# Kernel optimization log

Measured on AMD Instinct MI355X. Metric: run time of the kernel, lower is better.

The kernel has to match this reference:

```python
import jax, jax.numpy as jnp
import numpy as np

N = 100_000   # total nodes across all subgraphs in batch
E = 1_600_000 # edges (avg degree 16)
B = 1_000     # number of subgraphs
D = 128       # in_dim = out_dim
SZ = N // B   # nodes per subgraph


def setup_inputs() -> dict:
    key = jax.random.key(0)
    ks = jax.random.split(key, 8)
    feat = jax.random.normal(ks[0], (N, D), dtype=jnp.float32)
    edge_src = jax.random.randint(ks[1], (E,), 0, N, dtype=jnp.int32)
    edge_dst = jax.random.randint(ks[2], (E,), 0, N, dtype=jnp.int32)
    # pre-normalized edge weights (is_normed=True path)
    edge_w = jax.random.uniform(ks[3], (E,), dtype=jnp.float32)
    s = 1.0 / np.sqrt(D)
    W1 = jax.random.normal(ks[4], (D, D), dtype=jnp.float32) * s
    W2 = jax.random.normal(ks[5], (D, D), dtype=jnp.float32) * s
    Wp = jax.random.normal(ks[6], (D, D), dtype=jnp.float32) * s
    b1 = jnp.zeros((D,), jnp.float32)
    b2 = jnp.zeros((D,), jnp.float32)
    bp = jnp.zeros((D,), jnp.float32)
    # contiguous equal-size subgraphs; target = first node of each subgraph
    seg_ids = jnp.repeat(jnp.arange(B, dtype=jnp.int32), SZ)
    target = jnp.arange(B, dtype=jnp.int32) * SZ
    size_subg = jnp.full((B,), float(SZ), jnp.float32)
    return dict(feat=feat, edge_w=edge_w, W1=W1, b1=b1, W2=W2, b2=b2,
                Wp=Wp, bp=bp, size_subg=size_subg,
                edge_src=edge_src, edge_dst=edge_dst,
                seg_ids=seg_ids, target=target)


def _gcn_layer(x, src, dst, w, W, b):
    # sparse A_hat @ x : gather src features, weight, scatter-add into dst
    msg = x[src] * w[:, None]                       # [E, D]
    agg = jax.ops.segment_sum(msg, dst, num_segments=N)  # [N, D]
    return jax.nn.relu(agg @ W + b)


def reference(feat, edge_w, W1, b1, W2, b2, Wp, bp, size_subg,
              edge_src, edge_dst, seg_ids, target):
    # two stacked GCN layers (self.structure = [structure1, structure2])
    h1 = _gcn_layer(feat, edge_src, edge_dst, edge_w, W1, b1)
    h2 = _gcn_layer(h1, edge_src, edge_dst, edge_w, W2, b2)
    # ResPool: residual-sum over layer outputs, mean pool per subgraph,
    # add target-node embedding (residual), then linear + relu
    h = h1 + h2                                              # [N, D]
    pooled = jax.ops.segment_sum(h, seg_ids, num_segments=B)
    pooled = pooled / size_subg[:, None] + h[target]         # [B, D]
    emb = jax.nn.relu(pooled @ Wp + bp)
    # F.normalize(p=2, dim=1), eps=1e-12
    norm = jnp.sqrt(jnp.sum(emb * emb, axis=1, keepdims=True))
    emb = emb / jnp.maximum(norm, 1e-12)
    return emb  # EnsembleDummy just returns the single branch
```

## Files before the change

### kernel.cpp

```cpp
#include <hip/hip_runtime.h>

#define DD 128
#define CHUNK 4096
#define BSH 8
#define MAXBK 512
#define MAXCH 512
#define CAP 6144

typedef _Float16 half8 __attribute__((ext_vector_type(8)));
typedef _Float16 half4v __attribute__((ext_vector_type(4)));
typedef float floatx4 __attribute__((ext_vector_type(4)));
typedef float floatx2 __attribute__((ext_vector_type(2)));

__global__ __launch_bounds__(256) void k_prep(const float* __restrict__ W1,
                                              _Float16* __restrict__ W1t,
                                              const float* __restrict__ W2,
                                              _Float16* __restrict__ W2t) {
    int idx = blockIdx.x * 256 + threadIdx.x;
    const float* W = (idx < DD * DD) ? W1 : W2;
    _Float16* Wt = (idx < DD * DD) ? W1t : W2t;
    int id = idx & (DD * DD - 1);
    int n = id >> 7, k = id & 127;
    Wt[n * DD + k] = (_Float16)W[k * DD + n];
}

__global__ __launch_bounds__(512) void k_histg1(const int* __restrict__ dst,
                                                int* __restrict__ histT,
                                                int E, int nChunks,
                                                const float* __restrict__ A,
                                                const _Float16* __restrict__ Wt,
                                                unsigned char* __restrict__ Y, int nrows) {
    if (blockIdx.x < nChunks) {
        __shared__ int lhist[MAXBK];
        int tid = threadIdx.x;
        lhist[tid] = 0;
        __syncthreads();
        int beg = blockIdx.x * CHUNK;
        int end = min(beg + CHUNK, E);
        for (int k = beg + tid; k < end; k += 512)
            atomicAdd(&lhist[dst[k] >> BSH], 1);
        __syncthreads();
        histT[tid * MAXCH + blockIdx.x] = lhist[tid];
    } else {
        int gblk = blockIdx.x - nChunks;
        int wave = threadIdx.x >> 6;
        int lane = threadIdx.x & 63;
        int row0 = gblk * 256 + wave * 32;
        int m = lane & 15;
        int q = lane >> 4;
        int r0 = min(row0 + m, nrows - 1);
        int r1 = min(row0 + 16 + m, nrows - 1);

        floatx4 acc[2][8];
        #pragma unroll
        for (int t = 0; t < 2; ++t)
            #pragma unroll
            for (int c = 0; c < 8; ++c)
                acc[t][c] = (floatx4){0.f, 0.f, 0.f, 0.f};

        #pragma unroll
        for (int ks = 0; ks < 4; ++ks) {
            int kbase = ks * 32 + q * 8;
            float4 x0 = *reinterpret_cast<const float4*>(A + (size_t)r0 * DD + kbase);
            float4 x1 = *reinterpret_cast<const float4*>(A + (size_t)r0 * DD + kbase + 4);
            float4 y0 = *reinterpret_cast<const float4*>(A + (size_t)r1 * DD + kbase);
            float4 y1 = *reinterpret_cast<const float4*>(A + (size_t)r1 * DD + kbase + 4);
            half8 a0, a1;
            a0[0]=(_Float16)x0.x; a0[1]=(_Float16)x0.y; a0[2]=(_Float16)x0.z; a0[3]=(_Float16)x0.w;
            a0[4]=(_Float16)x1.x; a0[5]=(_Float16)x1.y; a0[6]=(_Float16)x1.z; a0[7]=(_Float16)x1.w;
            a1[0]=(_Float16)y0.x; a1[1]=(_Float16)y0.y; a1[2]=(_Float16)y0.z; a1[3]=(_Float16)y0.w;
            a1[4]=(_Float16)y1.x; a1[5]=(_Float16)y1.y; a1[6]=(_Float16)y1.z; a1[7]=(_Float16)y1.w;
            #pragma unroll
            for (int c = 0; c < 8; ++c) {
                half8 b = *reinterpret_cast<const half8*>(Wt + (size_t)(c * 16 + m) * DD + kbase);
                acc[0][c] = __builtin_amdgcn_mfma_f32_16x16x32_f16(b, a0, acc[0][c], 0, 0, 0);
                acc[1][c] = __builtin_amdgcn_mfma_f32_16x16x32_f16(b, a1, acc[1][c], 0, 0, 0);
            }
        }

        #pragma unroll
        for (int t = 0; t < 2; ++t) {
            int row = row0 + t * 16 + m;
            if (row >= nrows) continue;
            size_t rb = (size_t)row * DD;
            #pragma unroll
            for (int c = 0; c < 8; ++c) {
                int col = c * 16 + q * 4;
                int u = 0;
                u = __builtin_amdgcn_cvt_pk_fp8_f32(acc[t][c][0], acc[t][c][1], u, false);
                u = __builtin_amdgcn_cvt_pk_fp8_f32(acc[t][c][2], acc[t][c][3], u, true);
                *reinterpret_cast<unsigned int*>(&Y[rb + col]) = (unsigned int)u;
            }
        }
    }
}

__global__ __launch_bounds__(512) void k_scan(int* __restrict__ histT,
                                              int* __restrict__ gcur, int nChunks) {
    __shared__ int wsum[8];
    int b = blockIdx.x;
    int c = threadIdx.x;
    int v = (c < nChunks) ? histT[b * MAXCH + c] : 0;
    int lane = c & 63, wave = c >> 6;
    int inc = v;
    #pragma unroll
    for (int off = 1; off < 64; off <<= 1) {
        int t = __shfl_up(inc, off, 64);
        if (lane >= off) inc += t;
    }
    if (lane == 63) wsum[wave] = inc;
    __syncthreads();
    if (c == 0) {
        int run = 0;
        #pragma unroll
        for (int j = 0; j < 8; ++j) { int t = wsum[j]; wsum[j] = run; run += t; }
    }
    __syncthreads();
    int ex = inc - v + wsum[wave];
    if (c < nChunks) histT[b * MAXCH + c] = ex;
    if (c == nChunks - 1) gcur[b] = ex + v;
}

__global__ __launch_bounds__(512) void k_pass1(const int* __restrict__ src,
                                               const int* __restrict__ dst,
                                               const float* __restrict__ w,
                                               const int* __restrict__ histT,
                                               int2* __restrict__ out, int E, int NB) {
    __shared__ int2 stg[CHUNK];
    __shared__ unsigned short bok[CHUNK];
    __shared__ int lhist[MAXBK];
    __shared__ int loff[MAXBK];
    __shared__ int lbase[MAXBK];
    __shared__ int lcur[MAXBK];
    int tid = threadIdx.x;
    lhist[tid] = 0;
    __syncthreads();

    int beg = blockIdx.x * CHUNK;
    int end = min(beg + CHUNK, E);
    for (int k = beg + tid; k < end; k += 512)
        atomicAdd(&lhist[dst[k] >> BSH], 1);
    __syncthreads();
    if (tid < 64) {
        int base = tid * 8, v[8], s = 0;
        #pragma unroll
        for (int j = 0; j < 8; ++j) { v[j] = lhist[base + j]; s += v[j]; }
        int scn = s;
        #pragma unroll
        for (int off = 1; off < 64; off <<= 1) {
            int t = __shfl_up(scn, off, 64);
            if (tid >= off) scn += t;
        }
        int ex = scn - s;
        #pragma unroll
        for (int j = 0; j < 8; ++j) { loff[base + j] = ex; lcur[base + j] = ex; ex += v[j]; }
    }
    __syncthreads();
    if (tid < NB)
        lbase[tid] = tid * CAP + histT[tid * MAXCH + blockIdx.x];
    for (int k = beg + tid; k < end; k += 512) {
        int d = dst[k];
        int b = d >> BSH;
        int p = atomicAdd(&lcur[b], 1);
        stg[p] = make_int2(src[k] | ((d & ((1 << BSH) - 1)) << 17),
                           __float_as_int(w[k]));
        bok[p] = (unsigned short)b;
    }
    __syncthreads();
    int total = end - beg;
    for (int j = tid; j < total; j += 512) {
        int b = bok[j];
        out[lbase[b] + (j - loff[b])] = stg[j];
    }
}

__global__ __launch_bounds__(512) void k_pass2(const int2* __restrict__ bkt,
                                               const int* __restrict__ gcur,
                                               int2* __restrict__ rows,
                                               int2* __restrict__ edges, int N) {
    __shared__ int lhist[1 << BSH];
    __shared__ int loff[1 << BSH];
    __shared__ int lcur[1 << BSH];
    int tid = threadIdx.x;
    int b = blockIdx.x;
    int base = b * CAP;
    int nrec = gcur[b];
    int d0 = b << BSH;

    if (tid < (1 << BSH)) lhist[tid] = 0;
    __syncthreads();
    for (int i = tid; i < nrec; i += 512)
        atomicAdd(&lhist[(unsigned)bkt[base + i].x >> 17], 1);
    __syncthreads();
    if (tid < 64) {
        int bs = tid * 4, vv[4], s = 0;
        #pragma unroll
        for (int j = 0; j < 4; ++j) { vv[j] = lhist[bs + j]; s += vv[j]; }
        int scn = s;
        #pragma unroll
        for (int off = 1; off < 64; off <<= 1) {
            int t = __shfl_up(scn, off, 64);
            if (tid >= off) scn += t;
        }
        int ex = scn - s;
        #pragma unroll
        for (int j = 0; j < 4; ++j) {
            loff[bs + j] = ex; lcur[bs + j] = ex; ex += vv[j];
        }
    }
    __syncthreads();
    if (tid < (1 << BSH)) {
        int d = d0 + tid;
        if (d < N)
            rows[d] = make_int2(base + loff[tid], base + loff[tid] + lhist[tid]);
    }
    for (int i = tid; i < nrec; i += 512) {
        int2 r = bkt[base + i];
        int dl = (unsigned)r.x >> 17;
        int p = base + atomicAdd(&lcur[dl], 1);
        edges[p] = make_int2(r.x & 0x1FFFF, r.y);
    }
}

__global__ __launch_bounds__(256) void k_gemm_f16A(const _Float16* __restrict__ A,
                                                   const _Float16* __restrict__ Wt,
                                                   unsigned char* __restrict__ Y,
                                                   int nrows) {
    int wave = threadIdx.x >> 6;
    int lane = threadIdx.x & 63;
    int row0 = blockIdx.x * 128 + wave * 32;
    int m = lane & 15;
    int q = lane >> 4;

    floatx4 acc[2][8];
    #pragma unroll
    for (int t = 0; t < 2; ++t)
        #pragma unroll
        for (int c = 0; c < 8; ++c)
            acc[t][c] = (floatx4){0.f, 0.f, 0.f, 0.f};

    #pragma unroll
    for (int ks = 0; ks < 4; ++ks) {
        int kbase = ks * 32 + q * 8;
        half8 a0 = *reinterpret_cast<const half8*>(A + (size_t)(row0 + m) * DD + kbase);
        half8 a1 = *reinterpret_cast<const half8*>(A + (size_t)(row0 + 16 + m) * DD + kbase);
        #pragma unroll
        for (int c = 0; c < 8; ++c) {
            half8 b = *reinterpret_cast<const half8*>(Wt + (size_t)(c * 16 + m) * DD + kbase);
            acc[0][c] = __builtin_amdgcn_mfma_f32_16x16x32_f16(b, a0, acc[0][c], 0, 0, 0);
            acc[1][c] = __builtin_amdgcn_mfma_f32_16x16x32_f16(b, a1, acc[1][c], 0, 0, 0);
        }
    }

    #pragma unroll
    for (int t = 0; t < 2; ++t) {
        int row = row0 + t * 16 + m;
        if (row >= nrows) continue;
        size_t rb = (size_t)row * DD;
        #pragma unroll
        for (int c = 0; c < 8; ++c) {
            int col = c * 16 + q * 4;
            int u = 0;
            u = __builtin_amdgcn_cvt_pk_fp8_f32(acc[t][c][0], acc[t][c][1], u, false);
            u = __builtin_amdgcn_cvt_pk_fp8_f32(acc[t][c][2], acc[t][c][3], u, true);
            *reinterpret_cast<unsigned int*>(&Y[rb + col]) = (unsigned int)u;
        }
    }
}

template<int U>
__device__ __forceinline__ void agg_batch(const unsigned char* __restrict__ x,
                                          const int2* __restrict__ edges,
                                          int base, int end, int lastIdx,
                                          int g, int sl, floatx2* acc2) {
    int2 e[U]; int ok[U];
    #pragma unroll
    for (int u = 0; u < U; ++u) {
        int idx = base + u * 4 + g;
        ok[u] = idx < end;
        e[u] = edges[min(idx, lastIdx)];
    }
    uint4 v[U];
    #pragma unroll
    for (int u = 0; u < U; ++u) {
        int row = ok[u] ? e[u].x : 0;
        v[u] = *reinterpret_cast<const uint4*>(x + (size_t)row * DD + sl * 16);
    }
    #pragma unroll
    for (int u = 0; u < U; ++u) {
        float wv = ok[u] ? __int_as_float(e[u].y) : 0.f;
        floatx2 w2 = (floatx2){wv, wv};
        acc2[0] += __builtin_amdgcn_cvt_pk_f32_fp8((int)v[u].x, false) * w2;
        acc2[1] += __builtin_amdgcn_cvt_pk_f32_fp8((int)v[u].x, true)  * w2;
        acc2[2] += __builtin_amdgcn_cvt_pk_f32_fp8((int)v[u].y, false) * w2;
        acc2[3] += __builtin_amdgcn_cvt_pk_f32_fp8((int)v[u].y, true)  * w2;
        acc2[4] += __builtin_amdgcn_cvt_pk_f32_fp8((int)v[u].z, false) * w2;
        acc2[5] += __builtin_amdgcn_cvt_pk_f32_fp8((int)v[u].z, true)  * w2;
        acc2[6] += __builtin_amdgcn_cvt_pk_f32_fp8((int)v[u].w, false) * w2;
        acc2[7] += __builtin_amdgcn_cvt_pk_f32_fp8((int)v[u].w, true)  * w2;
    }
}

__global__ __launch_bounds__(256) void k_agg_eplg(const unsigned char* __restrict__ x,
                                                  const int2* __restrict__ rows,
                                                  const int2* __restrict__ edges,
                                                  const float* __restrict__ bias,
                                                  const _Float16* __restrict__ resid,
                                                  _Float16* __restrict__ out, int N) {
    int gwave = (blockIdx.x * blockDim.x + threadIdx.x) >> 6;
    int lane = threadIdx.x & 63;
    int half = lane >> 5;
    int hl = lane & 31;
    int wid = gwave * 2 + half;
    if (wid >= N) return;
    int g = hl >> 3;
    int sl = hl & 7;
    int2 rr = rows[wid];
    int beg = rr.x, end = rr.y;
    int lastIdx = max(end - 1, beg);
    floatx2 acc2[8];
    #pragma unroll
    for (int j = 0; j < 8; ++j) acc2[j] = (floatx2){0.f, 0.f};

    agg_batch<8>(x, edges, beg, end, lastIdx, g, sl, acc2);
    for (int i = beg + 32; i < end; i += 16)
        agg_batch<4>(x, edges, i, end, lastIdx, g, sl, acc2);

    #pragma unroll
    for (int j = 0; j < 8; ++j) {
        acc2[j][0] += __shfl_xor(acc2[j][0], 8, 64);
        acc2[j][1] += __shfl_xor(acc2[j][1], 8, 64);
        acc2[j][0] += __shfl_xor(acc2[j][0], 16, 64);
        acc2[j][1] += __shfl_xor(acc2[j][1], 16, 64);
    }
    if (g == 0) {
        float acc[16];
        #pragma unroll
        for (int j = 0; j < 8; ++j) { acc[2 * j] = acc2[j][0]; acc[2 * j + 1] = acc2[j][1]; }
        size_t rb = (size_t)wid * DD + sl * 16;
        float bb[16];
        #pragma unroll
        for (int q = 0; q < 4; ++q) {
            float4 b4 = *reinterpret_cast<const float4*>(&bias[sl * 16 + q * 4]);
            bb[q * 4 + 0] = b4.x; bb[q * 4 + 1] = b4.y;
            bb[q * 4 + 2] = b4.z; bb[q * 4 + 3] = b4.w;
        }
        half8 o0, o1;
        if (resid) {
            half8 r0 = *reinterpret_cast<const half8*>(&resid[rb]);
            half8 r1 = *reinterpret_cast<const half8*>(&resid[rb + 8]);
            #pragma unroll
            for (int j = 0; j < 8; ++j) {
                float v = acc[j] + bb[j];
                v = v > 0.f ? v : 0.f;
                o0[j] = (_Float16)(v + (float)r0[j]);
            }
            #pragma unroll
            for (int j = 0; j < 8; ++j) {
                float v = acc[8 + j] + bb[8 + j];
                v = v > 0.f ? v : 0.f;
                o1[j] = (_Float16)(v + (float)r1[j]);
            }
        } else {
            #pragma unroll
            for (int j = 0; j < 8; ++j) {
                float v = acc[j] + bb[j];
                o0[j] = (_Float16)(v > 0.f ? v : 0.f);
            }
            #pragma unroll
            for (int j = 0; j < 8; ++j) {
                float v = acc[8 + j] + bb[8 + j];
                o1[j] = (_Float16)(v > 0.f ? v : 0.f);
            }
        }
        *reinterpret_cast<half8*>(&out[rb]) = o0;
        *reinterpret_cast<half8*>(&out[rb + 8]) = o1;
    }
}

__global__ __launch_bounds__(256) void k_pool_final(const _Float16* __restrict__ h,
                                                    const int* __restrict__ target,
                                                    const float* __restrict__ size_subg,
                                                    const float* __restrict__ Wp,
                                                    const float* __restrict__ bp,
                                                    float* __restrict__ out, int SZ) {
    __shared__ float part[16][DD];
    __shared__ float p[DD];
    __shared__ float wsum[2];
    int b = blockIdx.x;
    int t = threadIdx.x;
    int c = t & 15;
    int r = t >> 4;
    const _Float16* hp = h + (size_t)b * SZ * DD;
    float s[8] = {0.f, 0.f, 0.f, 0.f, 0.f, 0.f, 0.f, 0.f};
    for (int n = r; n < SZ; n += 16) {
        half8 v = *reinterpret_cast<const half8*>(hp + (size_t)n * DD + c * 8);
        #pragma unroll
        for (int j = 0; j < 8; ++j) s[j] += (float)v[j];
    }
    #pragma unroll
    for (int j = 0; j < 8; ++j) part[r][c * 8 + j] = s[j];
    __syncthreads();
    if (t < DD) {
        float sum = 0.f;
        #pragma unroll
        for (int rr = 0; rr < 16; ++rr) sum += part[rr][t];
        int tg = target[b];
        p[t] = sum / size_subg[b] + (float)h[(size_t)tg * DD + t];
    }
    __syncthreads();
    if (t < DD) {
        float acc = 0.f;
        #pragma unroll 4
        for (int k = 0; k < DD; ++k) acc = fmaf(p[k], Wp[k * DD + t], acc);
        float e = acc + bp[t];
        e = e > 0.f ? e : 0.f;
        float sq = e * e;
        #pragma unroll
        for (int off = 32; off > 0; off >>= 1) sq += __shfl_down(sq, off, 64);
        int lane = t & 63, w = t >> 6;
        if (lane == 0) wsum[w] = sq;
        __syncthreads();
        float norm = sqrtf(wsum[0] + wsum[1]);
        float scale = 1.f / fmaxf(norm, 1e-12f);
        out[b * DD + t] = e * scale;
    } else {
        __syncthreads();
    }
}

extern "C" void kernel_launch(void* const* d_in, const int* in_sizes, int n_in,
                              void* d_out, int out_size, void* d_ws, size_t ws_size,
                              hipStream_t stream) {
    const float* feat      = (const float*)d_in[0];
    const float* edge_w    = (const float*)d_in[1];
    const float* W1        = (const float*)d_in[2];
    const float* b1        = (const float*)d_in[3];
    const float* W2        = (const float*)d_in[4];
    const float* b2        = (const float*)d_in[5];
    const float* Wp        = (const float*)d_in[6];
    const float* bp        = (const float*)d_in[7];
    const float* size_subg = (const float*)d_in[8];
    const int*   edge_src  = (const int*)d_in[9];
    const int*   edge_dst  = (const int*)d_in[10];
    const int*   target    = (const int*)d_in[12];

    const int N  = in_sizes[0] / DD;
    const int E  = in_sizes[1];
    const int B  = in_sizes[8];
    const int SZ = N / B;

    const int P  = ((N + 127) / 128) * 128;
    const int NB = (N + (1 << BSH) - 1) >> BSH;
    const int nChunks = (E + CHUNK - 1) / CHUNK;

    char* ws = (char*)d_ws;
    size_t off = 0;
    auto alloc = [&](size_t bytes) {
        void* p = ws + off;
        off += (bytes + 255) & ~(size_t)255;
        return p;
    };
    unsigned char* Y = (unsigned char*)alloc((size_t)P * DD);
    _Float16* h1     = (_Float16*)alloc((size_t)P * DD * 2);
    _Float16* H      = (_Float16*)alloc((size_t)P * DD * 2);
    _Float16* W1t    = (_Float16*)alloc((size_t)DD * DD * 2);
    _Float16* W2t    = (_Float16*)alloc((size_t)DD * DD * 2);
    int2*  rows      = (int2*)alloc((size_t)N * 8);
    int*   gcur      = (int*)alloc((size_t)MAXBK * 4);
    int*   histT     = (int*)alloc((size_t)MAXBK * MAXCH * 4);
    int2*  edges_bkt = (int2*)alloc((size_t)NB * CAP * 8);
    int2*  edges     = (int2*)alloc((size_t)NB * CAP * 8);

    k_prep<<<128, 256, 0, stream>>>(W1, W1t, W2, W2t);

    int g1Blocks = (N + 255) / 256;
    k_histg1<<<nChunks + g1Blocks, 512, 0, stream>>>(
        edge_dst, histT, E, nChunks, feat, W1t, Y, N);

    k_scan<<<NB, 512, 0, stream>>>(histT, gcur, nChunks);

    k_pass1<<<nChunks, 512, 0, stream>>>(edge_src, edge_dst, edge_w, histT,
                                         edges_bkt, E, NB);

    k_pass2<<<NB, 512, 0, stream>>>(edges_bkt, gcur, rows, edges, N);

    int nodePairs  = (N + 1) / 2;
    int aggBlocks  = (nodePairs * 64 + 255) / 256;
    int gemmBlocks = (N + 127) / 128;

    k_agg_eplg<<<aggBlocks, 256, 0, stream>>>(Y, rows, edges, b1, nullptr, h1, N);
    k_gemm_f16A<<<gemmBlocks, 256, 0, stream>>>(h1, W2t, Y, N);
    k_agg_eplg<<<aggBlocks, 256, 0, stream>>>(Y, rows, edges, b2, h1, H, N);
    k_pool_final<<<B, 256, 0, stream>>>(H, target, size_subg, Wp, bp,
                                        (float*)d_out, SZ);
}
```

Baseline: 300.9 us.

## Co-schedule layer-1 GEMM with bucket scatter pass and force packed FMA

Moves the first-layer feature GEMM out of the histogram kernel and into the same launch as the bucket-scatter pass. The short histogram kernel now runs alone and the heavier scatter overlaps with the GEMM blocks. Separately, the aggregation inner loop uses inline-asm v_pk_fma_f32 instead of separate packed multiply and add. The fused kernel now carries the larger pass1 shared-memory footprint for GEMM blocks too, which may lower their occupancy. The inline asm also limits compiler scheduling.

```diff
diff --git a/kernel.cpp b/kernel.cpp
--- a/kernel.cpp
+++ b/kernel.cpp
@@ -11,6 +11,12 @@
 typedef _Float16 half4v __attribute__((ext_vector_type(4)));
 typedef float floatx4 __attribute__((ext_vector_type(4)));
 typedef float floatx2 __attribute__((ext_vector_type(2)));
+
+__device__ __forceinline__ floatx2 pk_fma(floatx2 a, floatx2 b, floatx2 c) {
+    floatx2 d;
+    asm("v_pk_fma_f32 %0, %1, %2, %3" : "=v"(d) : "v"(a), "v"(b), "v"(c));
+    return d;
+}
 
 __global__ __launch_bounds__(256) void k_prep(const float* __restrict__ W1,
                                               _Float16* __restrict__ W1t,
@@ -24,25 +30,104 @@
     Wt[n * DD + k] = (_Float16)W[k * DD + n];
 }
 
-__global__ __launch_bounds__(512) void k_histg1(const int* __restrict__ dst,
-                                                int* __restrict__ histT,
-                                                int E, int nChunks,
-                                                const float* __restrict__ A,
-                                                const _Float16* __restrict__ Wt,
-                                                unsigned char* __restrict__ Y, int nrows) {
-    if (blockIdx.x < nChunks) {
+__global__ __launch_bounds__(512) void k_hist(const int* __restrict__ dst,
+                                              int* __restrict__ histT, int E) {
+    __shared__ int lhist[MAXBK];
+    int tid = threadIdx.x;
+    lhist[tid] = 0;
+    __syncthreads();
+    int beg = blockIdx.x * CHUNK;
+    int end = min(beg + CHUNK, E);
+    for (int k = beg + tid; k < end; k += 512)
+        atomicAdd(&lhist[dst[k] >> BSH], 1);
+    __syncthreads();
+    histT[tid * MAXCH + blockIdx.x] = lhist[tid];
+}
+
+__global__ __launch_bounds__(512) void k_scan(int* __restrict__ histT,
+                                              int* __restrict__ gcur, int nChunks) {
+    __shared__ int wsum[8];
+    int b = blockIdx.x;
+    int c = threadIdx.x;
+    int v = (c < nChunks) ? histT[b * MAXCH + c] : 0;
+    int lane = c & 63, wave = c >> 6;
+    int inc = v;
+    #pragma unroll
+    for (int off = 1; off < 64; off <<= 1) {
+        int t = __shfl_up(inc, off, 64);
+        if (lane >= off) inc += t;
+    }
+    if (lane == 63) wsum[wave] = inc;
+    __syncthreads();
+    if (c == 0) {
+        int run = 0;
+        #pragma unroll
+        for (int j = 0; j < 8; ++j) { int t = wsum[j]; wsum[j] = run; run += t; }
+    }
+    __syncthreads();
+    int ex = inc - v + wsum[wave];
+    if (c < nChunks) histT[b * MAXCH + c] = ex;
+    if (c == nChunks - 1) gcur[b] = ex + v;
+}
+
+__global__ __launch_bounds__(512) void k_p1g1(const int* __restrict__ src,
+                                              const int* __restrict__ dst,
+                                              const float* __restrict__ w,
+                                              const int* __restrict__ histT,
+                                              int2* __restrict__ out, int E, int NB,
+                                              int p1Blocks,
+                                              const float* __restrict__ A,
+                                              const _Float16* __restrict__ Wt,
+                                              unsigned char* __restrict__ Y, int nrows) {
+    if (blockIdx.x < p1Blocks) {
+        __shared__ int2 stg[CHUNK];
+        __shared__ unsigned short bok[CHUNK];
         __shared__ int lhist[MAXBK];
+        __shared__ int loff[MAXBK];
+        __shared__ int lbase[MAXBK];
+        __shared__ int lcur[MAXBK];
         int tid = threadIdx.x;
         lhist[tid] = 0;
         __syncthreads();
+
         int beg = blockIdx.x * CHUNK;
         int end = min(beg + CHUNK, E);
         for (int k = beg + tid; k < end; k += 512)
             atomicAdd(&lhist[dst[k] >> BSH], 1);
         __syncthreads();
-        histT[tid * MAXCH + blockIdx.x] = lhist[tid];
+        if (tid < 64) {
+            int base = tid * 8, v[8], s = 0;
+            #pragma unroll
+            for (int j = 0; j < 8; ++j) { v[j] = lhist[base + j]; s += v[j]; }
+            int scn = s;
+            #pragma unroll
+            for (int off = 1; off < 64; off <<= 1) {
+                int t = __shfl_up(scn, off, 64);
+                if (tid >= off) scn += t;
+            }
+            int ex = scn - s;
+            #pragma unroll
+            for (int j = 0; j < 8; ++j) { loff[base + j] = ex; lcur[base + j] = ex; ex += v[j]; }
+        }
+        __syncthreads();
+        if (tid < NB)
+            lbase[tid] = tid * CAP + histT[tid * MAXCH + blockIdx.x];
+        for (int k = beg + tid; k < end; k += 512) {
+            int d = dst[k];
+            int b = d >> BSH;
+            int p = atomicAdd(&lcur[b], 1);
+            stg[p] = make_int2(src[k] | ((d & ((1 << BSH) - 1)) << 17),
+                               __float_as_int(w[k]));
+            bok[p] = (unsigned short)b;
+        }
+        __syncthreads();
+        int total = end - beg;
+        for (int j = tid; j < total; j += 512) {
+            int b = bok[j];
+            out[lbase[b] + (j - loff[b])] = stg[j];
+        }
     } else {
-        int gblk = blockIdx.x - nChunks;
+        int gblk = blockIdx.x - p1Blocks;
         int wave = threadIdx.x >> 6;
         int lane = threadIdx.x & 63;
         int row0 = gblk * 256 + wave * 32;
@@ -92,85 +177,6 @@
                 *reinterpret_cast<unsigned int*>(&Y[rb + col]) = (unsigned int)u;
             }
         }
-    }
-}
-
-__global__ __launch_bounds__(512) void k_scan(int* __restrict__ histT,
-                                              int* __restrict__ gcur, int nChunks) {
-    __shared__ int wsum[8];
-    int b = blockIdx.x;
-    int c = threadIdx.x;
-    int v = (c < nChunks) ? histT[b * MAXCH + c] : 0;
-    int lane = c & 63, wave = c >> 6;
-    int inc = v;
-    #pragma unroll
-    for (int off = 1; off < 64; off <<= 1) {
-        int t = __shfl_up(inc, off, 64);
-        if (lane >= off) inc += t;
-    }
-    if (lane == 63) wsum[wave] = inc;
-    __syncthreads();
-    if (c == 0) {
-        int run = 0;
-        #pragma unroll
-        for (int j = 0; j < 8; ++j) { int t = wsum[j]; wsum[j] = run; run += t; }
-    }
-    __syncthreads();
-    int ex = inc - v + wsum[wave];
-    if (c < nChunks) histT[b * MAXCH + c] = ex;
-    if (c == nChunks - 1) gcur[b] = ex + v;
-}
-
-__global__ __launch_bounds__(512) void k_pass1(const int* __restrict__ src,
-                                               const int* __restrict__ dst,
-                                               const float* __restrict__ w,
-                                               const int* __restrict__ histT,
-                                               int2* __restrict__ out, int E, int NB) {
-    __shared__ int2 stg[CHUNK];
-    __shared__ unsigned short bok[CHUNK];
-    __shared__ int lhist[MAXBK];
-    __shared__ int loff[MAXBK];
-    __shared__ int lbase[MAXBK];
-    __shared__ int lcur[MAXBK];
-    int tid = threadIdx.x;
-    lhist[tid] = 0;
-    __syncthreads();
-
-    int beg = blockIdx.x * CHUNK;
-    int end = min(beg + CHUNK, E);
-    for (int k = beg + tid; k < end; k += 512)
-        atomicAdd(&lhist[dst[k] >> BSH], 1);
-    __syncthreads();
-    if (tid < 64) {
-        int base = tid * 8, v[8], s = 0;
-        #pragma unroll
-        for (int j = 0; j < 8; ++j) { v[j] = lhist[base + j]; s += v[j]; }
-        int scn = s;
-        #pragma unroll
-        for (int off = 1; off < 64; off <<= 1) {
-            int t = __shfl_up(scn, off, 64);
-            if (tid >= off) scn += t;
-        }
-        int ex = scn - s;
-        #pragma unroll
-        for (int j = 0; j < 8; ++j) { loff[base + j] = ex; lcur[base + j] = ex; ex += v[j]; }
-    }
-    __syncthreads();
-    if (tid < NB)
-        lbase[tid] = tid * CAP + histT[tid * MAXCH + blockIdx.x];
-    for (int k = beg + tid; k < end; k += 512) {
-        int d = dst[k];
-        int b = d >> BSH;
-        int p = atomicAdd(&lcur[b], 1);
-        stg[p] = make_int2(src[k] | ((d & ((1 << BSH) - 1)) << 17),
-                           __float_as_int(w[k]));
-        bok[p] = (unsigned short)b;
-    }
-    __syncthreads();
-    int total = end - beg;
-    for (int j = tid; j < total; j += 512) {
-        int b = bok[j];
-        out[lbase[b] + (j - loff[b])] = stg[j];
     }
 }
 
@@ -290,14 +296,14 @@
     for (int u = 0; u < U; ++u) {
         float wv = ok[u] ? __int_as_float(e[u].y) : 0.f;
         floatx2 w2 = (floatx2){wv, wv};
-        acc2[0] += __builtin_amdgcn_cvt_pk_f32_fp8((int)v[u].x, false) * w2;
-        acc2[1] += __builtin_amdgcn_cvt_pk_f32_fp8((int)v[u].x, true)  * w2;
-        acc2[2] += __builtin_amdgcn_cvt_pk_f32_fp8((int)v[u].y, false) * w2;
-        acc2[3] += __builtin_amdgcn_cvt_pk_f32_fp8((int)v[u].y, true)  * w2;
-        acc2[4] += __builtin_amdgcn_cvt_pk_f32_fp8((int)v[u].z, false) * w2;
-        acc2[5] += __builtin_amdgcn_cvt_pk_f32_fp8((int)v[u].z, true)  * w2;
-        acc2[6] += __builtin_amdgcn_cvt_pk_f32_fp8((int)v[u].w, false) * w2;
-        acc2[7] += __builtin_amdgcn_cvt_pk_f32_fp8((int)v[u].w, true)  * w2;
+        acc2[0] = pk_fma(__builtin_amdgcn_cvt_pk_f32_fp8((int)v[u].x, false), w2, acc2[0]);
+        acc2[1] = pk_fma(__builtin_amdgcn_cvt_pk_f32_fp8((int)v[u].x, true),  w2, acc2[1]);
+        acc2[2] = pk_fma(__builtin_amdgcn_cvt_pk_f32_fp8((int)v[u].y, false), w2, acc2[2]);
+        acc2[3] = pk_fma(__builtin_amdgcn_cvt_pk_f32_fp8((int)v[u].y, true),  w2, acc2[3]);
+        acc2[4] = pk_fma(__builtin_amdgcn_cvt_pk_f32_fp8((int)v[u].z, false), w2, acc2[4]);
+        acc2[5] = pk_fma(__builtin_amdgcn_cvt_pk_f32_fp8((int)v[u].z, true),  w2, acc2[5]);
+        acc2[6] = pk_fma(__builtin_amdgcn_cvt_pk_f32_fp8((int)v[u].w, false), w2, acc2[6]);
+        acc2[7] = pk_fma(__builtin_amdgcn_cvt_pk_f32_fp8((int)v[u].w, true),  w2, acc2[7]);
     }
 }
 
@@ -474,14 +480,14 @@
 
     k_prep<<<128, 256, 0, stream>>>(W1, W1t, W2, W2t);
 
+    k_hist<<<nChunks, 512, 0, stream>>>(edge_dst, histT, E);
+
+    k_scan<<<NB, 512, 0, stream>>>(histT, gcur, nChunks);
+
     int g1Blocks = (N + 255) / 256;
-    k_histg1<<<nChunks + g1Blocks, 512, 0, stream>>>(
-        edge_dst, histT, E, nChunks, feat, W1t, Y, N);
-
-    k_scan<<<NB, 512, 0, stream>>>(histT, gcur, nChunks);
-
-    k_pass1<<<nChunks, 512, 0, stream>>>(edge_src, edge_dst, edge_w, histT,
-                                         edges_bkt, E, NB);
+    k_p1g1<<<nChunks + g1Blocks, 512, 0, stream>>>(
+        edge_src, edge_dst, edge_w, histT, edges_bkt, E, NB, nChunks,
+        feat, W1t, Y, N);
 
     k_pass2<<<NB, 512, 0, stream>>>(edges_bkt, gcur, rows, edges, N);
 
```

Result: no change. 305.6 us (+1.6%).
